# Performance work log

Hardware: AMD Instinct MI355X
Metric: run time of the kernel (lower is better)

## Reference

```python
import jax, jax.numpy as jnp
import numpy as np

EPS = 1e-5  # BatchNorm eps (eval mode, uses running stats)


def _conv1x1(x, W, b):
    # x: [B,C,H,W], W: [O,C], b: [O] -> [B,O,H,W]
    return jnp.einsum('bchw,oc->bohw', x, W) + b[None, :, None, None]


def setup_inputs() -> dict:
    key = jax.random.key(0)
    ks = jax.random.split(key, 13)
    B, C, M, N = 16, 512, 64, 64
    CR = C // 2
    s = 0.02
    return {
        'x': jax.random.normal(ks[0], (B, C, M, N), dtype=jnp.float32),
        'Wq': jax.random.normal(ks[1], (CR, C), dtype=jnp.float32) * s,
        'bq': jax.random.normal(ks[2], (CR,), dtype=jnp.float32) * s,
        'Wk': jax.random.normal(ks[3], (CR, C), dtype=jnp.float32) * s,
        'bk': jax.random.normal(ks[4], (CR,), dtype=jnp.float32) * s,
        'Wv': jax.random.normal(ks[5], (CR, C), dtype=jnp.float32) * s,
        'bv': jax.random.normal(ks[6], (CR,), dtype=jnp.float32) * s,
        'Wr': jax.random.normal(ks[7], (C, CR), dtype=jnp.float32) * s,
        'br': jax.random.normal(ks[8], (C,), dtype=jnp.float32) * s,
        'gamma': jax.random.normal(ks[9], (C,), dtype=jnp.float32) * 0.1 + 1.0,
        'beta': jax.random.normal(ks[10], (C,), dtype=jnp.float32) * 0.1,
        'running_mean': jax.random.normal(ks[11], (C,), dtype=jnp.float32) * 0.1,
        'running_var': jax.random.uniform(ks[12], (C,), dtype=jnp.float32, minval=0.5, maxval=1.5),
    }


def reference(x, Wq, bq, Wk, bk, Wv, bv, Wr, br, gamma, beta, running_mean, running_var):
    b, c, m, n = x.shape
    cr = Wq.shape[0]
    # 1x1-conv QKV projections
    Q = _conv1x1(x, Wq, bq).reshape(b * cr, m, n)
    K = _conv1x1(x, Wk, bk).reshape(b * cr, m, n)
    V = _conv1x1(x, Wv, bv).reshape(b * cr, m, n)
    # per-channel spatial attention over rows: [b*cr, m, m]
    corr = jnp.einsum('gik,gjk->gij', Q, K)
    attn = jax.nn.softmax(corr, axis=-1)
    y = jnp.einsum('gij,gjn->gin', attn, V).reshape(b, cr, m, n)
    # reconstruct: 1x1 conv + BatchNorm (eval mode) + residual
    y = _conv1x1(y, Wr, br)
    inv = gamma / jnp.sqrt(running_var + EPS)
    y = y * inv[None, :, None, None] + (beta - running_mean * inv)[None, :, None, None]
    return y + x
```

## Files before the change

### kernel.cpp

```cpp
#include <hip/hip_runtime.h>

typedef __attribute__((ext_vector_type(8))) short bf16x8;
typedef __attribute__((ext_vector_type(4))) float f32x4;

#define DEVI static __device__ __forceinline__

DEVI unsigned short f2b(float f) {
  union { float f; unsigned u; } v; v.f = f;
  unsigned r = v.u + 0x7fffu + ((v.u >> 16) & 1u);
  return (unsigned short)(r >> 16);
}

typedef const __attribute__((address_space(1))) void* gas1_t;
typedef __attribute__((address_space(3))) void* las3_t;
#define GL16(g, l) __builtin_amdgcn_global_load_lds((gas1_t)(g), (las3_t)(l), 16, 0, 0)

#define WAITVM(N) asm volatile("s_waitcnt vmcnt(" #N ")" ::: "memory")
#define WAITLGKM  asm volatile("s_waitcnt lgkmcnt(0)" ::: "memory")

#define OFF_WQKV  0ull
#define OFF_WR    786432ull
#define OFF_BQKV  1048576ull
#define OFF_SCALE 1051648ull
#define OFF_OFF2  1053696ull
#define OFF_XT    2097152ull
#define OFF_YT    2097152ull
#define OFF_Y     35651584ull
#define OFF_Q     69206016ull

__global__ __launch_bounds__(256) void k_prep(
    const float* __restrict__ Wq, const float* __restrict__ bq,
    const float* __restrict__ Wk, const float* __restrict__ bk,
    const float* __restrict__ Wv, const float* __restrict__ bv,
    const float* __restrict__ Wr, const float* __restrict__ br,
    const float* __restrict__ gamma, const float* __restrict__ beta,
    const float* __restrict__ rm, const float* __restrict__ rv,
    unsigned short* __restrict__ wqkv, unsigned short* __restrict__ wrb,
    float* __restrict__ bqkv, float* __restrict__ scale, float* __restrict__ off2)
{
  int i = blockIdx.x * 256 + threadIdx.x;
  if (i < 768 * 512) {
    int o = i >> 9, c = i & 511;
    float v = (o < 256) ? Wq[o * 512 + c] : (o < 512 ? Wk[(o - 256) * 512 + c] : Wv[(o - 512) * 512 + c]);
    wqkv[i] = f2b(v);
  }
  if (i < 512 * 256) wrb[i] = f2b(Wr[i]);
  if (i < 768) bqkv[i] = (i < 256) ? bq[i] : (i < 512 ? bk[i - 256] : bv[i - 512]);
  if (i < 512) {
    float inv = gamma[i] * rsqrtf(rv[i] + 1e-5f);
    scale[i] = inv;
    off2[i] = (br[i] - rm[i]) * inv + beta[i];
  }
}

__global__ __launch_bounds__(256) void k_xt(const float* __restrict__ x, unsigned short* __restrict__ xt)
{
  __shared__ unsigned short tile[64][72];
  const int b = blockIdx.z, c0 = blockIdx.y * 64, s0 = blockIdx.x * 64;
  const int t = threadIdx.x;
  const int r = t >> 2, cc = (t & 3) * 16;
  const float* src = x + ((size_t)b * 512 + c0 + r) * 4096 + s0 + cc;
  #pragma unroll
  for (int j = 0; j < 16; j += 4) {
    float4 v = *(const float4*)(src + j);
    tile[r][cc + j + 0] = f2b(v.x);
    tile[r][cc + j + 1] = f2b(v.y);
    tile[r][cc + j + 2] = f2b(v.z);
    tile[r][cc + j + 3] = f2b(v.w);
  }
  __syncthreads();
  unsigned short* dst = xt + ((size_t)b * 4096 + s0 + r) * 512 + c0 + cc;
  bf16x8 o0, o1;
  #pragma unroll
  for (int j = 0; j < 8; ++j) { o0[j] = tile[cc + j][r]; o1[j] = tile[cc + 8 + j][r]; }
  *(bf16x8*)(dst) = o0;
  *(bf16x8*)(dst + 8) = o1;
}

__global__ __launch_bounds__(256) void k_qkv(
    const unsigned short* __restrict__ xt, const unsigned short* __restrict__ wqkv,
    const float* __restrict__ bqkv, unsigned short* __restrict__ qkv)
{
  __shared__ unsigned short lds[4][2][4096];
  const int b = blockIdx.z, o0 = blockIdx.y * 128, s0 = blockIdx.x * 128;
  const int t = threadIdx.x, w = t >> 6, l = t & 63;
  const int wm = w >> 1, wn = w & 1, lr = l & 15, koff = (l >> 4) * 8;

  const unsigned short* Ag = wqkv + (size_t)(o0 + (t >> 2)) * 512 + (t & 3) * 8;
  const unsigned short* Bg = xt + ((size_t)b * 4096 + s0 + (t >> 2)) * 512 + (t & 3) * 8;

  const f32x4 z = {0.f, 0.f, 0.f, 0.f};
  f32x4 acc[4][4];
  #pragma unroll
  for (int i = 0; i < 4; ++i)
    #pragma unroll
    for (int j = 0; j < 4; ++j) acc[i][j] = z;

#define STG_Q(st, kt) do { \
    GL16(Ag + (kt) * 32,            (char*)&lds[st][0][0] + t * 16); \
    GL16(Ag + (kt) * 32 + 64 * 512, (char*)&lds[st][0][0] + t * 16 + 4096); \
    GL16(Bg + (kt) * 32,            (char*)&lds[st][1][0] + t * 16); \
    GL16(Bg + (kt) * 32 + 64 * 512, (char*)&lds[st][1][0] + t * 16 + 4096); \
  } while (0)

#define CMP_Q(st) do { \
    const unsigned short* A  = &lds[st][0][0]; \
    const unsigned short* Bl = &lds[st][1][0]; \
    bf16x8 af[4], bfr[4]; \
    _Pragma("unroll") \
    for (int mi = 0; mi < 4; ++mi) af[mi] = *(const bf16x8*)(A + (wm * 64 + mi * 16 + lr) * 32 + koff); \
    _Pragma("unroll") \
    for (int ni = 0; ni < 4; ++ni) bfr[ni] = *(const bf16x8*)(Bl + (wn * 64 + ni * 16 + lr) * 32 + koff); \
    _Pragma("unroll") \
    for (int mi = 0; mi < 4; ++mi) \
      _Pragma("unroll") \
      for (int ni = 0; ni < 4; ++ni) \
        acc[mi][ni] = __builtin_amdgcn_mfma_f32_16x16x32_bf16(af[mi], bfr[ni], acc[mi][ni], 0, 0, 0); \
    WAITLGKM; __builtin_amdgcn_sched_barrier(0); \
  } while (0)

  STG_Q(0, 0); STG_Q(1, 1); STG_Q(2, 2);
  #pragma unroll
  for (int kt = 0; kt < 13; ++kt) {
    WAITVM(8);
    __builtin_amdgcn_s_barrier();
    STG_Q((kt + 3) & 3, kt + 3);
    CMP_Q(kt & 3);
  }
  WAITVM(8); __builtin_amdgcn_s_barrier(); CMP_Q(1);
  WAITVM(4); __builtin_amdgcn_s_barrier(); CMP_Q(2);
  WAITVM(0); __builtin_amdgcn_s_barrier(); CMP_Q(3);

  #pragma unroll
  for (int mi = 0; mi < 4; ++mi) {
    #pragma unroll
    for (int reg = 0; reg < 4; ++reg) {
      const int o = o0 + wm * 64 + mi * 16 + (l >> 4) * 4 + reg;
      const float bias = bqkv[o];
      const size_t base = (size_t)(o >> 8) * 16777216ull + ((size_t)b * 256 + (o & 255)) * 4096;
      #pragma unroll
      for (int ni = 0; ni < 4; ++ni) {
        const int s = s0 + wn * 64 + ni * 16 + lr;
        qkv[base + s] = f2b(acc[mi][ni][reg] + bias);
      }
    }
  }
#undef STG_Q
#undef CMP_Q
}

__global__ __launch_bounds__(256) void k_attn(const unsigned short* __restrict__ qkv,
                                              unsigned short* __restrict__ yout)
{
  __shared__ unsigned short Vt[64][80];
  __shared__ unsigned short P[4][16][80];
  const int g = blockIdx.x;
  const unsigned short* qg = qkv + (size_t)g * 4096;
  const unsigned short* kg = qkv + 16777216ull + (size_t)g * 4096;
  const unsigned short* vg = qkv + 33554432ull + (size_t)g * 4096;
  const int t = threadIdx.x, w = t >> 6, l = t & 63;
  const int lr = l & 15, lk = (l >> 4) * 8;

  {
    const int j = t >> 2, c0 = (t & 3) * 16;
    bf16x8 a = *(const bf16x8*)(vg + j * 64 + c0);
    bf16x8 bb = *(const bf16x8*)(vg + j * 64 + c0 + 8);
    #pragma unroll
    for (int jj = 0; jj < 8; ++jj) { Vt[c0 + jj][j] = a[jj]; Vt[c0 + 8 + jj][j] = bb[jj]; }
  }

  const f32x4 z = {0.f, 0.f, 0.f, 0.f};
  bf16x8 qf[2];
  #pragma unroll
  for (int kc = 0; kc < 2; ++kc) qf[kc] = *(const bf16x8*)(qg + (w * 16 + lr) * 64 + kc * 32 + lk);
  f32x4 accS[4] = {z, z, z, z};
  #pragma unroll
  for (int jt = 0; jt < 4; ++jt)
    #pragma unroll
    for (int kc = 0; kc < 2; ++kc) {
      bf16x8 kf = *(const bf16x8*)(kg + (jt * 16 + lr) * 64 + kc * 32 + lk);
      accS[jt] = __builtin_amdgcn_mfma_f32_16x16x32_bf16(qf[kc], kf, accS[jt], 0, 0, 0);
    }

  #pragma unroll
  for (int reg = 0; reg < 4; ++reg) {
    float mx = fmaxf(fmaxf(accS[0][reg], accS[1][reg]), fmaxf(accS[2][reg], accS[3][reg]));
    #pragma unroll
    for (int m = 1; m < 16; m <<= 1) mx = fmaxf(mx, __shfl_xor(mx, m, 64));
    float e0 = __expf(accS[0][reg] - mx), e1 = __expf(accS[1][reg] - mx);
    float e2 = __expf(accS[2][reg] - mx), e3 = __expf(accS[3][reg] - mx);
    float sm = e0 + e1 + e2 + e3;
    #pragma unroll
    for (int m = 1; m < 16; m <<= 1) sm += __shfl_xor(sm, m, 64);
    const float rs = 1.f / sm;
    const int row = (l >> 4) * 4 + reg;
    P[w][row][0 * 16 + lr] = f2b(e0 * rs);
    P[w][row][1 * 16 + lr] = f2b(e1 * rs);
    P[w][row][2 * 16 + lr] = f2b(e2 * rs);
    P[w][row][3 * 16 + lr] = f2b(e3 * rs);
  }
  __syncthreads();

  bf16x8 pf[2];
  #pragma unroll
  for (int kc = 0; kc < 2; ++kc) pf[kc] = *(const bf16x8*)(&P[w][lr][kc * 32 + lk]);
  f32x4 accY[4] = {z, z, z, z};
  #pragma unroll
  for (int nt = 0; nt < 4; ++nt)
    #pragma unroll
    for (int kc = 0; kc < 2; ++kc) {
      bf16x8 vf = *(const bf16x8*)(&Vt[nt * 16 + lr][kc * 32 + lk]);
      accY[nt] = __builtin_amdgcn_mfma_f32_16x16x32_bf16(pf[kc], vf, accY[nt], 0, 0, 0);
    }

  unsigned short* yg = yout + (size_t)g * 4096;
  #pragma unroll
  for (int nt = 0; nt < 4; ++nt)
    #pragma unroll
    for (int reg = 0; reg < 4; ++reg) {
      const int i = w * 16 + (l >> 4) * 4 + reg;
      yg[i * 64 + nt * 16 + lr] = f2b(accY[nt][reg]);
    }
}

__global__ __launch_bounds__(256) void k_yt(const unsigned short* __restrict__ y, unsigned short* __restrict__ yt)
{
  __shared__ unsigned short tile[64][72];
  const int b = blockIdx.z, cr0 = blockIdx.y * 64, s0 = blockIdx.x * 64;
  const int t = threadIdx.x, r = t >> 2, c0 = (t & 3) * 16;
  const unsigned short* src = y + ((size_t)b * 256 + cr0 + r) * 4096 + s0 + c0;
  bf16x8 a = *(const bf16x8*)(src);
  bf16x8 bb = *(const bf16x8*)(src + 8);
  #pragma unroll
  for (int j = 0; j < 8; ++j) { tile[r][c0 + j] = a[j]; tile[r][c0 + 8 + j] = bb[j]; }
  __syncthreads();
  unsigned short* dst = yt + ((size_t)b * 4096 + s0 + r) * 256 + cr0 + c0;
  bf16x8 o0, o1;
  #pragma unroll
  for (int j = 0; j < 8; ++j) { o0[j] = tile[c0 + j][r]; o1[j] = tile[c0 + 8 + j][r]; }
  *(bf16x8*)(dst) = o0;
  *(bf16x8*)(dst + 8) = o1;
}

__global__ __launch_bounds__(256) void k_recon(
    const unsigned short* __restrict__ yt, const unsigned short* __restrict__ wrb,
    const float* __restrict__ scale, const float* __restrict__ off2,
    const float* __restrict__ x, float* __restrict__ out)
{
  __shared__ unsigned short lds[4][2][4096];
  const int b = blockIdx.z, o0 = blockIdx.y * 128, s0 = blockIdx.x * 128;
  const int t = threadIdx.x, w = t >> 6, l = t & 63;
  const int wm = w >> 1, wn = w & 1, lr = l & 15, koff = (l >> 4) * 8;

  const unsigned short* Ag = wrb + (size_t)(o0 + (t >> 2)) * 256 + (t & 3) * 8;
  const unsigned short* Bg = yt + ((size_t)b * 4096 + s0 + (t >> 2)) * 256 + (t & 3) * 8;

  const f32x4 z = {0.f, 0.f, 0.f, 0.f};
  f32x4 acc[4][4];
  #pragma unroll
  for (int i = 0; i < 4; ++i)
    #pragma unroll
    for (int j = 0; j < 4; ++j) acc[i][j] = z;

#define STG_R(st, kt) do { \
    GL16(Ag + (kt) * 32,            (char*)&lds[st][0][0] + t * 16); \
    GL16(Ag + (kt) * 32 + 64 * 256, (char*)&lds[st][0][0] + t * 16 + 4096); \
    GL16(Bg + (kt) * 32,            (char*)&lds[st][1][0] + t * 16); \
    GL16(Bg + (kt) * 32 + 64 * 256, (char*)&lds[st][1][0] + t * 16 + 4096); \
  } while (0)

#define CMP_R(st) do { \
    const unsigned short* A  = &lds[st][0][0]; \
    const unsigned short* Bl = &lds[st][1][0]; \
    bf16x8 af[4], bfr[4]; \
    _Pragma("unroll") \
    for (int mi = 0; mi < 4; ++mi) af[mi] = *(const bf16x8*)(A + (wm * 64 + mi * 16 + lr) * 32 + koff); \
    _Pragma("unroll") \
    for (int ni = 0; ni < 4; ++ni) bfr[ni] = *(const bf16x8*)(Bl + (wn * 64 + ni * 16 + lr) * 32 + koff); \
    _Pragma("unroll") \
    for (int mi = 0; mi < 4; ++mi) \
      _Pragma("unroll") \
      for (int ni = 0; ni < 4; ++ni) \
        acc[mi][ni] = __builtin_amdgcn_mfma_f32_16x16x32_bf16(af[mi], bfr[ni], acc[mi][ni], 0, 0, 0); \
    WAITLGKM; __builtin_amdgcn_sched_barrier(0); \
  } while (0)

  STG_R(0, 0); STG_R(1, 1); STG_R(2, 2);
  #pragma unroll
  for (int kt = 0; kt < 5; ++kt) {
    WAITVM(8);
    __builtin_amdgcn_s_barrier();
    STG_R((kt + 3) & 3, kt + 3);
    CMP_R(kt & 3);
  }
  WAITVM(8); __builtin_amdgcn_s_barrier(); CMP_R(1);
  WAITVM(4); __builtin_amdgcn_s_barrier(); CMP_R(2);
  WAITVM(0); __builtin_amdgcn_s_barrier(); CMP_R(3);

  #pragma unroll
  for (int mi = 0; mi < 4; ++mi) {
    #pragma unroll
    for (int reg = 0; reg < 4; ++reg) {
      const int o = o0 + wm * 64 + mi * 16 + (l >> 4) * 4 + reg;
      const float sc = scale[o], of = off2[o];
      const size_t base = ((size_t)b * 512 + o) * 4096;
      #pragma unroll
      for (int ni = 0; ni < 4; ++ni) {
        const int s = s0 + wn * 64 + ni * 16 + lr;
        const size_t idx = base + s;
        out[idx] = acc[mi][ni][reg] * sc + of + x[idx];
      }
    }
  }
#undef STG_R
#undef CMP_R
}

extern "C" void kernel_launch(void* const* d_in, const int* in_sizes, int n_in,
                              void* d_out, int out_size, void* d_ws, size_t ws_size,
                              hipStream_t stream)
{
  const float* x     = (const float*)d_in[0];
  const float* Wq    = (const float*)d_in[1];
  const float* bq    = (const float*)d_in[2];
  const float* Wk    = (const float*)d_in[3];
  const float* bk    = (const float*)d_in[4];
  const float* Wv    = (const float*)d_in[5];
  const float* bv    = (const float*)d_in[6];
  const float* Wr    = (const float*)d_in[7];
  const float* br    = (const float*)d_in[8];
  const float* gamma = (const float*)d_in[9];
  const float* beta  = (const float*)d_in[10];
  const float* rm    = (const float*)d_in[11];
  const float* rv    = (const float*)d_in[12];

  char* ws = (char*)d_ws;
  unsigned short* wqkv  = (unsigned short*)(ws + OFF_WQKV);
  unsigned short* wrb   = (unsigned short*)(ws + OFF_WR);
  float* bqkv  = (float*)(ws + OFF_BQKV);
  float* scale = (float*)(ws + OFF_SCALE);
  float* off2  = (float*)(ws + OFF_OFF2);
  unsigned short* xt  = (unsigned short*)(ws + OFF_XT);
  unsigned short* yt  = (unsigned short*)(ws + OFF_YT);
  unsigned short* yb  = (unsigned short*)(ws + OFF_Y);
  unsigned short* qkv = (unsigned short*)(ws + OFF_Q);
  float* out = (float*)d_out;

  hipLaunchKernelGGL(k_prep, dim3(1536), dim3(256), 0, stream,
                     Wq, bq, Wk, bk, Wv, bv, Wr, br, gamma, beta, rm, rv,
                     wqkv, wrb, bqkv, scale, off2);
  hipLaunchKernelGGL(k_xt, dim3(64, 8, 16), dim3(256), 0, stream, x, xt);
  hipLaunchKernelGGL(k_qkv, dim3(32, 6, 16), dim3(256), 0, stream, xt, wqkv, bqkv, qkv);
  hipLaunchKernelGGL(k_attn, dim3(4096), dim3(256), 0, stream, qkv, yb);
  hipLaunchKernelGGL(k_yt, dim3(64, 4, 16), dim3(256), 0, stream, yb, yt);
  hipLaunchKernelGGL(k_recon, dim3(32, 4, 16), dim3(256), 0, stream, yt, wrb, scale, off2, x, out);
}
```

Before: 222.7 us.

## Use BK=64 double-buffered XOR-swizzled LDS tiles in projection GEMMs

Both the QKV and reconstruction GEMM kernels switch from a 4-stage pipeline with K-tiles of 32 to a 2-stage pipeline with K-tiles of 64, halving the number of barrier/wait iterations. LDS rows are now 128 bytes and use an XOR swizzle on the 16-byte chunk index, applied on the global-to-LDS load and on the fragment reads, to avoid bank conflicts. The cost is less prefetch depth (only one tile in flight ahead) and an extra barrier before each refill of a buffer.

```diff
diff --git a/kernel.cpp b/kernel.cpp
--- a/kernel.cpp
+++ b/kernel.cpp
@@ -77,17 +77,21 @@
   *(bf16x8*)(dst + 8) = o1;
 }
 
+
 __global__ __launch_bounds__(256) void k_qkv(
     const unsigned short* __restrict__ xt, const unsigned short* __restrict__ wqkv,
     const float* __restrict__ bqkv, unsigned short* __restrict__ qkv)
 {
-  __shared__ unsigned short lds[4][2][4096];
+  __shared__ unsigned short lds[2][2][8192];
   const int b = blockIdx.z, o0 = blockIdx.y * 128, s0 = blockIdx.x * 128;
   const int t = threadIdx.x, w = t >> 6, l = t & 63;
-  const int wm = w >> 1, wn = w & 1, lr = l & 15, koff = (l >> 4) * 8;
-
-  const unsigned short* Ag = wqkv + (size_t)(o0 + (t >> 2)) * 512 + (t & 3) * 8;
-  const unsigned short* Bg = xt + ((size_t)b * 4096 + s0 + (t >> 2)) * 512 + (t & 3) * 8;
+  const int wm = w >> 1, wn = w & 1, lr = l & 15;
+  const int lkE = (l >> 4) * 8;
+  const int swE = (lr & 7) * 8;
+  const int cp = (t & 7) ^ ((t >> 3) & 7);
+
+  const unsigned short* Ag = wqkv + (size_t)(o0 + (t >> 3)) * 512 + cp * 8;
+  const unsigned short* Bg = xt + ((size_t)b * 4096 + s0 + (t >> 3)) * 512 + cp * 8;
 
   const f32x4 z = {0.f, 0.f, 0.f, 0.f};
   f32x4 acc[4][4];
@@ -97,39 +101,47 @@
     for (int j = 0; j < 4; ++j) acc[i][j] = z;
 
 #define STG_Q(st, kt) do { \
-    GL16(Ag + (kt) * 32,            (char*)&lds[st][0][0] + t * 16); \
-    GL16(Ag + (kt) * 32 + 64 * 512, (char*)&lds[st][0][0] + t * 16 + 4096); \
-    GL16(Bg + (kt) * 32,            (char*)&lds[st][1][0] + t * 16); \
-    GL16(Bg + (kt) * 32 + 64 * 512, (char*)&lds[st][1][0] + t * 16 + 4096); \
+    _Pragma("unroll") \
+    for (int j = 0; j < 4; ++j) { \
+      GL16(Ag + (kt) * 64 + j * 32 * 512, (char*)&lds[st][0][0] + j * 4096 + t * 16); \
+      GL16(Bg + (kt) * 64 + j * 32 * 512, (char*)&lds[st][1][0] + j * 4096 + t * 16); \
+    } \
   } while (0)
 
 #define CMP_Q(st) do { \
     const unsigned short* A  = &lds[st][0][0]; \
     const unsigned short* Bl = &lds[st][1][0]; \
-    bf16x8 af[4], bfr[4]; \
     _Pragma("unroll") \
-    for (int mi = 0; mi < 4; ++mi) af[mi] = *(const bf16x8*)(A + (wm * 64 + mi * 16 + lr) * 32 + koff); \
-    _Pragma("unroll") \
-    for (int ni = 0; ni < 4; ++ni) bfr[ni] = *(const bf16x8*)(Bl + (wn * 64 + ni * 16 + lr) * 32 + koff); \
-    _Pragma("unroll") \
-    for (int mi = 0; mi < 4; ++mi) \
-      _Pragma("unroll") \
-      for (int ni = 0; ni < 4; ++ni) \
-        acc[mi][ni] = __builtin_amdgcn_mfma_f32_16x16x32_bf16(af[mi], bfr[ni], acc[mi][ni], 0, 0, 0); \
+    for (int kc = 0; kc < 2; ++kc) { \
+      const int kidx = (kc * 32 + lkE) ^ swE; \
+      bf16x8 af[4], bfr[4]; \
+      _Pragma("unroll") \
+      for (int mi = 0; mi < 4; ++mi) af[mi] = *(const bf16x8*)(A + (wm * 64 + mi * 16 + lr) * 64 + kidx); \
+      _Pragma("unroll") \
+      for (int ni = 0; ni < 4; ++ni) bfr[ni] = *(const bf16x8*)(Bl + (wn * 64 + ni * 16 + lr) * 64 + kidx); \
+      _Pragma("unroll") \
+      for (int mi = 0; mi < 4; ++mi) \
+        _Pragma("unroll") \
+        for (int ni = 0; ni < 4; ++ni) \
+          acc[mi][ni] = __builtin_amdgcn_mfma_f32_16x16x32_bf16(af[mi], bfr[ni], acc[mi][ni], 0, 0, 0); \
+    } \
     WAITLGKM; __builtin_amdgcn_sched_barrier(0); \
   } while (0)
 
-  STG_Q(0, 0); STG_Q(1, 1); STG_Q(2, 2);
-  #pragma unroll
-  for (int kt = 0; kt < 13; ++kt) {
+  STG_Q(0, 0); STG_Q(1, 1);
+  #pragma unroll
+  for (int kt = 0; kt < 7; ++kt) {
     WAITVM(8);
     __builtin_amdgcn_s_barrier();
-    STG_Q((kt + 3) & 3, kt + 3);
-    CMP_Q(kt & 3);
-  }
-  WAITVM(8); __builtin_amdgcn_s_barrier(); CMP_Q(1);
-  WAITVM(4); __builtin_amdgcn_s_barrier(); CMP_Q(2);
-  WAITVM(0); __builtin_amdgcn_s_barrier(); CMP_Q(3);
+    CMP_Q(kt & 1);
+    if (kt + 2 < 8) {
+      __builtin_amdgcn_s_barrier();
+      STG_Q(kt & 1, kt + 2);
+    }
+  }
+  WAITVM(0);
+  __builtin_amdgcn_s_barrier();
+  CMP_Q(1);
 
   #pragma unroll
   for (int mi = 0; mi < 4; ++mi) {
@@ -247,13 +259,16 @@
     const float* __restrict__ scale, const float* __restrict__ off2,
     const float* __restrict__ x, float* __restrict__ out)
 {
-  __shared__ unsigned short lds[4][2][4096];
+  __shared__ unsigned short lds[2][2][8192];
   const int b = blockIdx.z, o0 = blockIdx.y * 128, s0 = blockIdx.x * 128;
   const int t = threadIdx.x, w = t >> 6, l = t & 63;
-  const int wm = w >> 1, wn = w & 1, lr = l & 15, koff = (l >> 4) * 8;
-
-  const unsigned short* Ag = wrb + (size_t)(o0 + (t >> 2)) * 256 + (t & 3) * 8;
-  const unsigned short* Bg = yt + ((size_t)b * 4096 + s0 + (t >> 2)) * 256 + (t & 3) * 8;
+  const int wm = w >> 1, wn = w & 1, lr = l & 15;
+  const int lkE = (l >> 4) * 8;
+  const int swE = (lr & 7) * 8;
+  const int cp = (t & 7) ^ ((t >> 3) & 7);
+
+  const unsigned short* Ag = wrb + (size_t)(o0 + (t >> 3)) * 256 + cp * 8;
+  const unsigned short* Bg = yt + ((size_t)b * 4096 + s0 + (t >> 3)) * 256 + cp * 8;
 
   const f32x4 z = {0.f, 0.f, 0.f, 0.f};
   f32x4 acc[4][4];
@@ -263,39 +278,47 @@
     for (int j = 0; j < 4; ++j) acc[i][j] = z;
 
 #define STG_R(st, kt) do { \
-    GL16(Ag + (kt) * 32,            (char*)&lds[st][0][0] + t * 16); \
-    GL16(Ag + (kt) * 32 + 64 * 256, (char*)&lds[st][0][0] + t * 16 + 4096); \
-    GL16(Bg + (kt) * 32,            (char*)&lds[st][1][0] + t * 16); \
-    GL16(Bg + (kt) * 32 + 64 * 256, (char*)&lds[st][1][0] + t * 16 + 4096); \
+    _Pragma("unroll") \
+    for (int j = 0; j < 4; ++j) { \
+      GL16(Ag + (kt) * 64 + j * 32 * 256, (char*)&lds[st][0][0] + j * 4096 + t * 16); \
+      GL16(Bg + (kt) * 64 + j * 32 * 256, (char*)&lds[st][1][0] + j * 4096 + t * 16); \
+    } \
   } while (0)
 
 #define CMP_R(st) do { \
     const unsigned short* A  = &lds[st][0][0]; \
     const unsigned short* Bl = &lds[st][1][0]; \
-    bf16x8 af[4], bfr[4]; \
     _Pragma("unroll") \
-    for (int mi = 0; mi < 4; ++mi) af[mi] = *(const bf16x8*)(A + (wm * 64 + mi * 16 + lr) * 32 + koff); \
-    _Pragma("unroll") \
-    for (int ni = 0; ni < 4; ++ni) bfr[ni] = *(const bf16x8*)(Bl + (wn * 64 + ni * 16 + lr) * 32 + koff); \
-    _Pragma("unroll") \
-    for (int mi = 0; mi < 4; ++mi) \
-      _Pragma("unroll") \
-      for (int ni = 0; ni < 4; ++ni) \
-        acc[mi][ni] = __builtin_amdgcn_mfma_f32_16x16x32_bf16(af[mi], bfr[ni], acc[mi][ni], 0, 0, 0); \
+    for (int kc = 0; kc < 2; ++kc) { \
+      const int kidx = (kc * 32 + lkE) ^ swE; \
+      bf16x8 af[4], bfr[4]; \
+      _Pragma("unroll") \
+      for (int mi = 0; mi < 4; ++mi) af[mi] = *(const bf16x8*)(A + (wm * 64 + mi * 16 + lr) * 64 + kidx); \
+      _Pragma("unroll") \
+      for (int ni = 0; ni < 4; ++ni) bfr[ni] = *(const bf16x8*)(Bl + (wn * 64 + ni * 16 + lr) * 64 + kidx); \
+      _Pragma("unroll") \
+      for (int mi = 0; mi < 4; ++mi) \
+        _Pragma("unroll") \
+        for (int ni = 0; ni < 4; ++ni) \
+          acc[mi][ni] = __builtin_amdgcn_mfma_f32_16x16x32_bf16(af[mi], bfr[ni], acc[mi][ni], 0, 0, 0); \
+    } \
     WAITLGKM; __builtin_amdgcn_sched_barrier(0); \
   } while (0)
 
-  STG_R(0, 0); STG_R(1, 1); STG_R(2, 2);
-  #pragma unroll
-  for (int kt = 0; kt < 5; ++kt) {
+  STG_R(0, 0); STG_R(1, 1);
+  #pragma unroll
+  for (int kt = 0; kt < 3; ++kt) {
     WAITVM(8);
     __builtin_amdgcn_s_barrier();
-    STG_R((kt + 3) & 3, kt + 3);
-    CMP_R(kt & 3);
-  }
-  WAITVM(8); __builtin_amdgcn_s_barrier(); CMP_R(1);
-  WAITVM(4); __builtin_amdgcn_s_barrier(); CMP_R(2);
-  WAITVM(0); __builtin_amdgcn_s_barrier(); CMP_R(3);
+    CMP_R(kt & 1);
+    if (kt + 2 < 4) {
+      __builtin_amdgcn_s_barrier();
+      STG_R(kt & 1, kt + 2);
+    }
+  }
+  WAITVM(0);
+  __builtin_amdgcn_s_barrier();
+  CMP_R(1);
 
   #pragma unroll
   for (int mi = 0; mi < 4; ++mi) {
```

After: 212.5 us. -4.6%, faster.
